# Kernel optimization log

Hardware: AMD Instinct MI355X
Metric: run time of the kernel (lower is better)

The kernel has to match this reference:

```python
import jax, jax.numpy as jnp
import numpy as np

# Module config (matches init_kwargs)
B, S, H = 4, 4096, 1024      # batch, seq_len, hidden_size
M = 2048                     # expert_dim (mid dim of each expert FFN)
E = 16                       # num_experts
K = 2                        # top_k


def setup_inputs() -> dict:
    key = jax.random.key(0)
    ks = jax.random.split(key, 5)
    X = jax.random.normal(ks[0], (B, S, H), dtype=jnp.float32)
    # gate: Linear(H, E)
    Wg = jax.random.normal(ks[1], (H, E), dtype=jnp.float32) * 0.02
    bg = jnp.zeros((E,), dtype=jnp.float32)
    # stacked expert params: fc1 (H->M), fc2 (M->H)
    W1 = jax.random.normal(ks[2], (E, H, M), dtype=jnp.float32) * 0.02
    b1 = jnp.zeros((E, M), dtype=jnp.float32)
    W2 = jax.random.normal(ks[3], (E, M, H), dtype=jnp.float32) * 0.02
    b2 = jnp.zeros((E, H), dtype=jnp.float32)
    return {"X": X, "Wg": Wg, "bg": bg, "W1": W1, "b1": b1, "W2": W2, "b2": b2}


def reference(X, Wg, bg, W1, b1, W2, b2):
    Bs, Ss, Hs = X.shape
    Xf = X.reshape(-1, Hs)                          # [T, H], T = B*S
    T = Xf.shape[0]
    # gate -> softmax -> top-k -> renormalize (same math as torch.topk(softmax))
    probs = jax.nn.softmax(Xf @ Wg + bg, axis=-1)   # [T, E]
    top_w, top_idx = jax.lax.top_k(probs, K)        # [T, K]
    top_w = top_w / jnp.sum(top_w, axis=-1, keepdims=True)
    # per-token combine weight for each expert (0 if expert not selected)
    cw = jnp.zeros((T, E), dtype=Xf.dtype).at[jnp.arange(T)[:, None], top_idx].add(top_w)  # [T, E]

    # scan over experts: each expert runs on all tokens, masked by its combine weight.
    # Mathematically identical to the per-token loop: out[t] = sum_k w[t,k] * Expert[idx[t,k]](x[t])
    def body(acc, xs):
        w1, bb1, w2, bb2, g = xs                    # g: [T] combine weights for this expert
        h = jax.nn.relu(Xf @ w1 + bb1)              # [T, M]
        acc = acc + g[:, None] * (h @ w2 + bb2)     # [T, H]
        return acc, None

    out, _ = jax.lax.scan(body, jnp.zeros_like(Xf), (W1, b1, W2, b2, cw.T))
    return out.reshape(Bs, Ss, Hs)
```

## Files before the change

kernel.cpp:

```cpp
#include <hip/hip_runtime.h>
#include <stdint.h>

#define T_TOK 16384
#define H_DIM 1024
#define M_DIM 2048
#define E_NUM 16

typedef __attribute__((ext_vector_type(8))) short bf16x8;
typedef __attribute__((ext_vector_type(4))) float f32x4;

#define GLOAD_LDS16(g, l) __builtin_amdgcn_global_load_lds( \
    (const __attribute__((address_space(1))) void*)(g),     \
    (__attribute__((address_space(3))) void*)(l), 16, 0, 0)

__device__ __forceinline__ ushort f2b(float f){ union{float f; unsigned i;} v; v.f=f; unsigned r=(v.i + 0x7fffu + ((v.i>>16)&1u))>>16; return (ushort)r; }

__global__ void k_detect(const ushort* X, int* flag){
  if (threadIdx.x == 0){
    int huge = 0;
    for (int i = 0; i < 256; i++){
      int ex = (X[i] >> 7) & 0xff;
      if (ex >= 200) huge = 1;
    }
    flag[0] = huge;
  }
}

__global__ void k_zero_fb(ushort* out, int n){
  int i = blockIdx.x * 256 + threadIdx.x;
  if (i < n) out[i] = 0;
}

__global__ __launch_bounds__(256) void k_zero(char* out, const int* flag, size_t half){
  size_t i = ((size_t)blockIdx.x * 256 + threadIdx.x) * 16;
  *(uint4*)(out + i) = make_uint4(0u,0u,0u,0u);
  if (flag[0] == 1) *(uint4*)(out + half + i) = make_uint4(0u,0u,0u,0u);
}

__global__ __launch_bounds__(256) void k_gate(const float* __restrict__ X,
    const float* __restrict__ Wg, const float* __restrict__ bg,
    float* __restrict__ top_w, int* __restrict__ pick,
    ushort* __restrict__ Xb, const int* __restrict__ flag)
{
  if (flag[0] != 1) return;
  int wave = threadIdx.x >> 6, lane = threadIdx.x & 63;
  int t0 = (blockIdx.x * 4 + wave) * 4;
  int equad = lane & 3, hgrp = lane >> 2;

  const float* x0 = X + (size_t)t0 * H_DIM;
  const float* x1 = x0 + H_DIM;
  const float* x2 = x1 + H_DIM;
  const float* x3 = x2 + H_DIM;

  float4 a0 = make_float4(0.f,0.f,0.f,0.f);
  float4 a1 = make_float4(0.f,0.f,0.f,0.f);
  float4 a2 = make_float4(0.f,0.f,0.f,0.f);
  float4 a3 = make_float4(0.f,0.f,0.f,0.f);

  #pragma unroll 4
  for (int hb = 0; hb < H_DIM / 16; hb++){
    int h = hb * 16 + hgrp;
    float4 w = *(const float4*)(Wg + h * E_NUM + equad * 4);
    float v0 = x0[h], v1 = x1[h], v2 = x2[h], v3 = x3[h];
    a0.x = fmaf(v0, w.x, a0.x); a0.y = fmaf(v0, w.y, a0.y); a0.z = fmaf(v0, w.z, a0.z); a0.w = fmaf(v0, w.w, a0.w);
    a1.x = fmaf(v1, w.x, a1.x); a1.y = fmaf(v1, w.y, a1.y); a1.z = fmaf(v1, w.z, a1.z); a1.w = fmaf(v1, w.w, a1.w);
    a2.x = fmaf(v2, w.x, a2.x); a2.y = fmaf(v2, w.y, a2.y); a2.z = fmaf(v2, w.z, a2.z); a2.w = fmaf(v2, w.w, a2.w);
    a3.x = fmaf(v3, w.x, a3.x); a3.y = fmaf(v3, w.y, a3.y); a3.z = fmaf(v3, w.z, a3.z); a3.w = fmaf(v3, w.w, a3.w);
  }

  #pragma unroll
  for (int off = 4; off <= 32; off <<= 1){
    a0.x += __shfl_xor(a0.x, off, 64); a0.y += __shfl_xor(a0.y, off, 64);
    a0.z += __shfl_xor(a0.z, off, 64); a0.w += __shfl_xor(a0.w, off, 64);
    a1.x += __shfl_xor(a1.x, off, 64); a1.y += __shfl_xor(a1.y, off, 64);
    a1.z += __shfl_xor(a1.z, off, 64); a1.w += __shfl_xor(a1.w, off, 64);
    a2.x += __shfl_xor(a2.x, off, 64); a2.y += __shfl_xor(a2.y, off, 64);
    a2.z += __shfl_xor(a2.z, off, 64); a2.w += __shfl_xor(a2.w, off, 64);
    a3.x += __shfl_xor(a3.x, off, 64); a3.y += __shfl_xor(a3.y, off, 64);
    a3.z += __shfl_xor(a3.z, off, 64); a3.w += __shfl_xor(a3.w, off, 64);
  }

  float lg0[16], lg1[16], lg2[16], lg3[16];
  #pragma unroll
  for (int g = 0; g < 4; g++){
    lg0[g*4+0] = __shfl(a0.x, g, 64); lg0[g*4+1] = __shfl(a0.y, g, 64);
    lg0[g*4+2] = __shfl(a0.z, g, 64); lg0[g*4+3] = __shfl(a0.w, g, 64);
    lg1[g*4+0] = __shfl(a1.x, g, 64); lg1[g*4+1] = __shfl(a1.y, g, 64);
    lg1[g*4+2] = __shfl(a1.z, g, 64); lg1[g*4+3] = __shfl(a1.w, g, 64);
    lg2[g*4+0] = __shfl(a2.x, g, 64); lg2[g*4+1] = __shfl(a2.y, g, 64);
    lg2[g*4+2] = __shfl(a2.z, g, 64); lg2[g*4+3] = __shfl(a2.w, g, 64);
    lg3[g*4+0] = __shfl(a3.x, g, 64); lg3[g*4+1] = __shfl(a3.y, g, 64);
    lg3[g*4+2] = __shfl(a3.z, g, 64); lg3[g*4+3] = __shfl(a3.w, g, 64);
  }
  #pragma unroll
  for (int e = 0; e < E_NUM; e++){
    float b = bg[e];
    lg0[e] += b; lg1[e] += b; lg2[e] += b; lg3[e] += b;
  }

  if (lane == 0){
    #pragma unroll
    for (int tk = 0; tk < 4; tk++){
      const float* lg = (tk == 0) ? lg0 : (tk == 1) ? lg1 : (tk == 2) ? lg2 : lg3;
      int t = t0 + tk;
      int i1 = 0; float m1 = lg[0];
      #pragma unroll
      for (int e = 1; e < E_NUM; e++) if (lg[e] > m1){ m1 = lg[e]; i1 = e; }
      int i2 = -1; float m2 = -1e30f;
      #pragma unroll
      for (int e = 0; e < E_NUM; e++) if (e != i1 && lg[e] > m2){ m2 = lg[e]; i2 = e; }
      if (i2 < 0) i2 = (i1 + 1) & 15;
      float e2 = __expf(m2 - m1);
      float w1 = 1.f / (1.f + e2);
      top_w[t*2]   = w1;
      top_w[t*2+1] = 1.f - w1;
      pick[t] = i1 | (i2 << 8);
    }
  }

  #pragma unroll
  for (int tk = 0; tk < 4; tk++){
    const float* xr = X + (size_t)(t0 + tk) * H_DIM;
    ushort* xb = Xb + (size_t)(t0 + tk) * H_DIM;
    #pragma unroll
    for (int hb = 0; hb < 4; hb++){
      int idx = hb * 256 + lane * 4;
      float4 v = *(const float4*)(xr + idx);
      ushort4 u;
      u.x = f2b(v.x); u.y = f2b(v.y); u.z = f2b(v.z); u.w = f2b(v.w);
      *(ushort4*)(xb + idx) = u;
    }
  }
}

__global__ __launch_bounds__(256) void k_bucket(const int* __restrict__ pick,
    int* __restrict__ cnt, int* __restrict__ bucket, const int* __restrict__ flag)
{
  if (flag[0] != 1) return;
  int e = blockIdx.x;
  int tid = threadIdx.x, lane = tid & 63, wave = tid >> 6;
  __shared__ int wsum[4];
  int running = 0;
  for (int c0 = 0; c0 < T_TOK; c0 += 256){
    int t = c0 + tid;
    int pk = pick[t];
    int val = -1;
    if ((pk & 0xff) == e) val = t * 2;
    else if (((pk >> 8) & 0xff) == e) val = t * 2 + 1;
    unsigned long long m = __ballot(val >= 0);
    int myidx = __popcll(m & ((1ull << lane) - 1ull));
    if (lane == 0) wsum[wave] = __popcll(m);
    __syncthreads();
    int wbase = 0;
    #pragma unroll
    for (int w = 0; w < 4; w++) if (w < wave) wbase += wsum[w];
    int tot = wsum[0] + wsum[1] + wsum[2] + wsum[3];
    if (val >= 0) bucket[e * T_TOK + running + wbase + myidx] = val;
    running += tot;
    __syncthreads();
  }
  if (tid == 0) cnt[e] = running;
}

__global__ void k_sched(const int* cnt, int* scan, int* ntl, int2* desc, const int* flag){
  if (threadIdx.x == 0){
    if (flag[0] != 1){ ntl[0] = 0; return; }
    int rowacc = 0, tot = 0;
    for (int e = 0; e < E_NUM; e++){
      scan[e] = rowacc; int c = cnt[e]; rowacc += c;
      int nt = (c + 127) >> 7;
      for (int t = 0; t < nt && tot < 384; t++){ desc[tot] = make_int2(e, t); tot++; }
    }
    ntl[0] = tot;
  }
}

__global__ __launch_bounds__(256) void k_transpose_cvt(const float* __restrict__ src,
                                                       ushort* __restrict__ dst,
                                                       int R, int C, const int* flag)
{
  if (flag[0] != 1) return;
  __shared__ ushort tile[64][68];
  int e = blockIdx.z;
  src += (size_t)e * R * C; dst += (size_t)e * R * C;
  int c0 = blockIdx.x * 64, r0 = blockIdx.y * 64;
  int tc = (threadIdx.x & 15) * 4, tr = threadIdx.x >> 4;
  #pragma unroll
  for (int p = 0; p < 4; p++){
    int r = tr + p * 16;
    float4 v = *(const float4*)&src[(size_t)(r0 + r) * C + (c0 + tc)];
    tile[r][tc] = f2b(v.x); tile[r][tc+1] = f2b(v.y); tile[r][tc+2] = f2b(v.z); tile[r][tc+3] = f2b(v.w);
  }
  __syncthreads();
  #pragma unroll
  for (int p = 0; p < 4; p++){
    int c = tr + p * 16;
    ushort4 v;
    v.x = tile[tc+0][c]; v.y = tile[tc+1][c]; v.z = tile[tc+2][c]; v.w = tile[tc+3][c];
    *(ushort4*)&dst[(size_t)(c0 + c) * R + (r0 + tc)] = v;
  }
}

__global__ __launch_bounds__(256) void k_fc1(
    const ushort* __restrict__ X, const ushort* __restrict__ W1t,
    const float* __restrict__ b1, ushort* __restrict__ h,
    const int* __restrict__ cnt, const int* __restrict__ scan,
    const int* __restrict__ ntl, const int2* __restrict__ desc,
    const int* __restrict__ bucket)
{
  if ((int)blockIdx.y >= ntl[0]) return;
  int2 d = desc[blockIdx.y];
  int e = d.x, tIdx = d.y;
  int c = cnt[e], sE = scan[e];
  int row0 = tIdx * 128, n0 = blockIdx.x * 128;

  __shared__ ushort As[128 * 64];
  __shared__ ushort Bs[128 * 64];
  __shared__ int rowTok[128];

  int tid = threadIdx.x, lane = tid & 63, wave = tid >> 6;
  if (tid < 128){
    int i = row0 + tid; int ic = i < c ? i : c - 1;
    rowTok[tid] = bucket[e * T_TOK + ic] >> 1;
  }
  __syncthreads();

  const char* aBase[4]; const char* bBase[4];
  #pragma unroll
  for (int cc = 0; cc < 4; cc++){
    int chunk = wave * 256 + cc * 64 + lane;
    int r = chunk >> 3, j = chunk & 7, jd = j ^ (r & 7);
    int tok = rowTok[r];
    aBase[cc] = (const char*)X + ((size_t)tok * H_DIM) * 2 + jd * 16;
    bBase[cc] = (const char*)W1t + ((size_t)(e * M_DIM + n0 + r) * H_DIM) * 2 + jd * 16;
  }

  f32x4 acc[4][4];
  #pragma unroll
  for (int mt = 0; mt < 4; mt++)
    #pragma unroll
    for (int nt = 0; nt < 4; nt++) acc[mt][nt] = (f32x4){0.f, 0.f, 0.f, 0.f};

  int wm = (wave >> 1) * 64, wn = (wave & 1) * 64;
  int col = lane & 15, quad = lane >> 4;

  for (int k0 = 0; k0 < H_DIM; k0 += 64){
    #pragma unroll
    for (int cc = 0; cc < 4; cc++){
      GLOAD_LDS16(aBase[cc] + k0 * 2, As + (wave * 256 + cc * 64) * 8);
      GLOAD_LDS16(bBase[cc] + k0 * 2, Bs + (wave * 256 + cc * 64) * 8);
    }
    __syncthreads();
    #pragma unroll
    for (int ks = 0; ks < 2; ks++){
      int jdA = (ks * 4 + quad) ^ (col & 7);
      bf16x8 af[4], bfr[4];
      #pragma unroll
      for (int mt = 0; mt < 4; mt++)
        af[mt] = *(const bf16x8*)&As[(wm + mt * 16 + col) * 64 + jdA * 8];
      #pragma unroll
      for (int nt = 0; nt < 4; nt++)
        bfr[nt] = *(const bf16x8*)&Bs[(wn + nt * 16 + col) * 64 + jdA * 8];
      #pragma unroll
      for (int mt = 0; mt < 4; mt++)
        #pragma unroll
        for (int nt = 0; nt < 4; nt++)
          acc[mt][nt] = __builtin_amdgcn_mfma_f32_16x16x32_bf16(af[mt], bfr[nt], acc[mt][nt], 0, 0, 0);
    }
    __syncthreads();
  }

  float bias[4];
  #pragma unroll
  for (int nt = 0; nt < 4; nt++) bias[nt] = b1[e * M_DIM + n0 + wn + nt * 16 + col];
  #pragma unroll
  for (int mt = 0; mt < 4; mt++){
    #pragma unroll
    for (int reg = 0; reg < 4; reg++){
      int ml = wm + mt * 16 + quad * 4 + reg;
      int i = row0 + ml;
      if (i < c){
        size_t base = (size_t)(sE + i) * M_DIM + n0 + wn + col;
        #pragma unroll
        for (int nt = 0; nt < 4; nt++){
          float v = acc[mt][nt][reg] + bias[nt];
          v = v > 0.f ? v : 0.f;
          h[base + nt * 16] = f2b(v);
        }
      }
    }
  }
}

__global__ __launch_bounds__(256) void k_fc2(
    const ushort* __restrict__ hbuf, const ushort* __restrict__ W2t,
    const float* __restrict__ b2, const float* __restrict__ top_w,
    float* __restrict__ out,
    const int* __restrict__ cnt, const int* __restrict__ scan,
    const int* __restrict__ ntl, const int2* __restrict__ desc,
    const int* __restrict__ bucket)
{
  if ((int)blockIdx.y >= ntl[0]) return;
  int2 d = desc[blockIdx.y];
  int e = d.x, tIdx = d.y;
  int c = cnt[e], sE = scan[e];
  int row0 = tIdx * 128, n0 = blockIdx.x * 128;

  __shared__ ushort As[128 * 64];
  __shared__ ushort Bs[128 * 64];
  __shared__ int rowLds[128];
  __shared__ float wLds[128];

  int tid = threadIdx.x, lane = tid & 63, wave = tid >> 6;
  if (tid < 128){
    int i = row0 + tid; int ic = i < c ? i : c - 1;
    int pk = bucket[e * T_TOK + ic];
    rowLds[tid] = pk >> 1; wLds[tid] = top_w[pk];
  }
  __syncthreads();

  const char* aBase[4]; const char* bBase[4];
  #pragma unroll
  for (int cc = 0; cc < 4; cc++){
    int chunk = wave * 256 + cc * 64 + lane;
    int r = chunk >> 3, j = chunk & 7, jd = j ^ (r & 7);
    int i = row0 + r; int ic = i < c ? i : c - 1;
    aBase[cc] = (const char*)hbuf + ((size_t)(sE + ic) * M_DIM) * 2 + jd * 16;
    bBase[cc] = (const char*)W2t + ((size_t)(e * H_DIM + n0 + r) * M_DIM) * 2 + jd * 16;
  }

  f32x4 acc[4][4];
  #pragma unroll
  for (int mt = 0; mt < 4; mt++)
    #pragma unroll
    for (int nt = 0; nt < 4; nt++) acc[mt][nt] = (f32x4){0.f, 0.f, 0.f, 0.f};

  int wm = (wave >> 1) * 64, wn = (wave & 1) * 64;
  int col = lane & 15, quad = lane >> 4;

  for (int k0 = 0; k0 < M_DIM; k0 += 64){
    #pragma unroll
    for (int cc = 0; cc < 4; cc++){
      GLOAD_LDS16(aBase[cc] + k0 * 2, As + (wave * 256 + cc * 64) * 8);
      GLOAD_LDS16(bBase[cc] + k0 * 2, Bs + (wave * 256 + cc * 64) * 8);
    }
    __syncthreads();
    #pragma unroll
    for (int ks = 0; ks < 2; ks++){
      int jdA = (ks * 4 + quad) ^ (col & 7);
      bf16x8 af[4], bfr[4];
      #pragma unroll
      for (int mt = 0; mt < 4; mt++)
        af[mt] = *(const bf16x8*)&As[(wm + mt * 16 + col) * 64 + jdA * 8];
      #pragma unroll
      for (int nt = 0; nt < 4; nt++)
        bfr[nt] = *(const bf16x8*)&Bs[(wn + nt * 16 + col) * 64 + jdA * 8];
      #pragma unroll
      for (int mt = 0; mt < 4; mt++)
        #pragma unroll
        for (int nt = 0; nt < 4; nt++)
          acc[mt][nt] = __builtin_amdgcn_mfma_f32_16x16x32_bf16(af[mt], bfr[nt], acc[mt][nt], 0, 0, 0);
    }
    __syncthreads();
  }

  float bias[4];
  #pragma unroll
  for (int nt = 0; nt < 4; nt++) bias[nt] = b2[e * H_DIM + n0 + wn + nt * 16 + col];
  #pragma unroll
  for (int mt = 0; mt < 4; mt++){
    #pragma unroll
    for (int reg = 0; reg < 4; reg++){
      int ml = wm + mt * 16 + quad * 4 + reg;
      int i = row0 + ml;
      if (i < c){
        int trow = rowLds[ml];
        float w = wLds[ml];
        size_t base = (size_t)trow * H_DIM + n0 + wn + col;
        #pragma unroll
        for (int nt = 0; nt < 4; nt++){
          float v = (acc[mt][nt][reg] + bias[nt]) * w;
          atomicAdd(&out[base + nt * 16], v);
        }
      }
    }
  }
}

extern "C" void kernel_launch(void* const* d_in, const int* in_sizes, int n_in,
                              void* d_out, int out_size, void* d_ws, size_t ws_size,
                              hipStream_t stream)
{
  const float* X  = (const float*)d_in[0];
  const float* Wg = (const float*)d_in[1];
  const float* bg = (const float*)d_in[2];
  const float* W1 = (const float*)d_in[3];
  const float* b1 = (const float*)d_in[4];
  const float* W2 = (const float*)d_in[5];
  const float* b2 = (const float*)d_in[6];
  float* out = (float*)d_out;

  const size_t AUX_SZ  = 2097152;
  const size_t XBF_SZ  = (size_t)T_TOK * H_DIM * 2;
  const size_t HBUF_SZ = (size_t)2 * T_TOK * M_DIM * 2;
  const size_t WT_SZ   = (size_t)E_NUM * H_DIM * M_DIM * 2;
  const size_t NEEDED  = AUX_SZ + XBF_SZ + HBUF_SZ + WT_SZ;

  if (ws_size < NEEDED){
    k_zero_fb<<<(out_size + 255) / 256, 256, 0, stream>>>((ushort*)d_out, out_size);
    return;
  }

  char* ws = (char*)d_ws;
  int*  cnt    = (int*)(ws);
  int*  scan   = (int*)(ws + 256);
  int*  ntl    = (int*)(ws + 512);
  int*  flag   = (int*)(ws + 768);
  int2* desc   = (int2*)(ws + 1024);
  float* topw  = (float*)(ws + 4096);
  int*  bucket = (int*)(ws + 139264);
  int*  pick   = (int*)(ws + 1572864);
  ushort* Xbf  = (ushort*)(ws + AUX_SZ);
  ushort* hbuf = (ushort*)(ws + AUX_SZ + XBF_SZ);
  ushort* Wt   = (ushort*)(ws + AUX_SZ + XBF_SZ + HBUF_SZ);

  k_detect<<<1, 64, 0, stream>>>((const ushort*)d_in[0], flag);
  k_zero<<<out_size / 2048, 256, 0, stream>>>((char*)d_out, flag, (size_t)out_size * 2);
  k_gate<<<1024, 256, 0, stream>>>(X, Wg, bg, topw, pick, Xbf, flag);
  k_bucket<<<E_NUM, 256, 0, stream>>>(pick, cnt, bucket, flag);
  k_sched<<<1, 64, 0, stream>>>(cnt, scan, ntl, desc, flag);
  k_transpose_cvt<<<dim3(32, 16, 16), 256, 0, stream>>>(W1, Wt, 1024, 2048, flag);
  k_fc1<<<dim3(16, 272), 256, 0, stream>>>(Xbf, Wt, b1, hbuf, cnt, scan, ntl, desc, bucket);
  k_transpose_cvt<<<dim3(16, 32, 16), 256, 0, stream>>>(W2, Wt, 2048, 1024, flag);
  k_fc2<<<dim3(8, 272), 256, 0, stream>>>(hbuf, Wt, b2, topw, out, cnt, scan, ntl, desc, bucket);
}
```

Baseline: 979.2 us.

## Double-buffer LDS tiles in expert GEMMs to overlap global loads with MFMA

Both expert GEMM kernels now use two LDS buffers per operand and prefetch the next K-slice with global_load_lds while MFMAs run on the current slice, with one waitcnt plus barrier per iteration. This targets the load latency that the single-buffer loop exposed between its two syncthreads. The per-block row index and weight LDS tables are removed: token indices and combine weights are now read directly from global memory per thread. LDS use doubles to 64KB per block, which may lower occupancy, and the direct gathers add redundant global reads.

```diff
diff --git a/kernel.cpp b/kernel.cpp
--- a/kernel.cpp
+++ b/kernel.cpp
@@ -214,23 +214,20 @@
   int c = cnt[e], sE = scan[e];
   int row0 = tIdx * 128, n0 = blockIdx.x * 128;
 
-  __shared__ ushort As[128 * 64];
-  __shared__ ushort Bs[128 * 64];
-  __shared__ int rowTok[128];
+  __shared__ ushort As[2][128 * 64];
+  __shared__ ushort Bs[2][128 * 64];
 
   int tid = threadIdx.x, lane = tid & 63, wave = tid >> 6;
-  if (tid < 128){
-    int i = row0 + tid; int ic = i < c ? i : c - 1;
-    rowTok[tid] = bucket[e * T_TOK + ic] >> 1;
-  }
-  __syncthreads();
 
   const char* aBase[4]; const char* bBase[4];
+  int ldsOff[4];
   #pragma unroll
   for (int cc = 0; cc < 4; cc++){
     int chunk = wave * 256 + cc * 64 + lane;
     int r = chunk >> 3, j = chunk & 7, jd = j ^ (r & 7);
-    int tok = rowTok[r];
+    int i = row0 + r; int ic = i < c ? i : c - 1;
+    int tok = bucket[e * T_TOK + ic] >> 1;
+    ldsOff[cc] = chunk * 8;
     aBase[cc] = (const char*)X + ((size_t)tok * H_DIM) * 2 + jd * 16;
     bBase[cc] = (const char*)W1t + ((size_t)(e * M_DIM + n0 + r) * H_DIM) * 2 + jd * 16;
   }
@@ -244,30 +241,43 @@
   int wm = (wave >> 1) * 64, wn = (wave & 1) * 64;
   int col = lane & 15, quad = lane >> 4;
 
+  #pragma unroll
+  for (int cc = 0; cc < 4; cc++){
+    GLOAD_LDS16(aBase[cc], &As[0][ldsOff[cc]]);
+    GLOAD_LDS16(bBase[cc], &Bs[0][ldsOff[cc]]);
+  }
+  asm volatile("s_waitcnt vmcnt(0)" ::: "memory");
+  __builtin_amdgcn_s_barrier();
+
+  int cur = 0;
   for (int k0 = 0; k0 < H_DIM; k0 += 64){
-    #pragma unroll
-    for (int cc = 0; cc < 4; cc++){
-      GLOAD_LDS16(aBase[cc] + k0 * 2, As + (wave * 256 + cc * 64) * 8);
-      GLOAD_LDS16(bBase[cc] + k0 * 2, Bs + (wave * 256 + cc * 64) * 8);
-    }
-    __syncthreads();
+    int nxt = cur ^ 1;
+    if (k0 + 64 < H_DIM){
+      #pragma unroll
+      for (int cc = 0; cc < 4; cc++){
+        GLOAD_LDS16(aBase[cc] + (k0 + 64) * 2, &As[nxt][ldsOff[cc]]);
+        GLOAD_LDS16(bBase[cc] + (k0 + 64) * 2, &Bs[nxt][ldsOff[cc]]);
+      }
+    }
     #pragma unroll
     for (int ks = 0; ks < 2; ks++){
       int jdA = (ks * 4 + quad) ^ (col & 7);
       bf16x8 af[4], bfr[4];
       #pragma unroll
       for (int mt = 0; mt < 4; mt++)
-        af[mt] = *(const bf16x8*)&As[(wm + mt * 16 + col) * 64 + jdA * 8];
+        af[mt] = *(const bf16x8*)&As[cur][(wm + mt * 16 + col) * 64 + jdA * 8];
       #pragma unroll
       for (int nt = 0; nt < 4; nt++)
-        bfr[nt] = *(const bf16x8*)&Bs[(wn + nt * 16 + col) * 64 + jdA * 8];
+        bfr[nt] = *(const bf16x8*)&Bs[cur][(wn + nt * 16 + col) * 64 + jdA * 8];
       #pragma unroll
       for (int mt = 0; mt < 4; mt++)
         #pragma unroll
         for (int nt = 0; nt < 4; nt++)
           acc[mt][nt] = __builtin_amdgcn_mfma_f32_16x16x32_bf16(af[mt], bfr[nt], acc[mt][nt], 0, 0, 0);
     }
-    __syncthreads();
+    asm volatile("s_waitcnt vmcnt(0)" ::: "memory");
+    __builtin_amdgcn_s_barrier();
+    cur = nxt;
   }
 
   float bias[4];
@@ -306,25 +316,19 @@
   int c = cnt[e], sE = scan[e];
   int row0 = tIdx * 128, n0 = blockIdx.x * 128;
 
-  __shared__ ushort As[128 * 64];
-  __shared__ ushort Bs[128 * 64];
-  __shared__ int rowLds[128];
-  __shared__ float wLds[128];
+  __shared__ ushort As[2][128 * 64];
+  __shared__ ushort Bs[2][128 * 64];
 
   int tid = threadIdx.x, lane = tid & 63, wave = tid >> 6;
-  if (tid < 128){
-    int i = row0 + tid; int ic = i < c ? i : c - 1;
-    int pk = bucket[e * T_TOK + ic];
-    rowLds[tid] = pk >> 1; wLds[tid] = top_w[pk];
-  }
-  __syncthreads();
 
   const char* aBase[4]; const char* bBase[4];
+  int ldsOff[4];
   #pragma unroll
   for (int cc = 0; cc < 4; cc++){
     int chunk = wave * 256 + cc * 64 + lane;
     int r = chunk >> 3, j = chunk & 7, jd = j ^ (r & 7);
     int i = row0 + r; int ic = i < c ? i : c - 1;
+    ldsOff[cc] = chunk * 8;
     aBase[cc] = (const char*)hbuf + ((size_t)(sE + ic) * M_DIM) * 2 + jd * 16;
     bBase[cc] = (const char*)W2t + ((size_t)(e * H_DIM + n0 + r) * M_DIM) * 2 + jd * 16;
   }
@@ -338,30 +342,43 @@
   int wm = (wave >> 1) * 64, wn = (wave & 1) * 64;
   int col = lane & 15, quad = lane >> 4;
 
+  #pragma unroll
+  for (int cc = 0; cc < 4; cc++){
+    GLOAD_LDS16(aBase[cc], &As[0][ldsOff[cc]]);
+    GLOAD_LDS16(bBase[cc], &Bs[0][ldsOff[cc]]);
+  }
+  asm volatile("s_waitcnt vmcnt(0)" ::: "memory");
+  __builtin_amdgcn_s_barrier();
+
+  int cur = 0;
   for (int k0 = 0; k0 < M_DIM; k0 += 64){
-    #pragma unroll
-    for (int cc = 0; cc < 4; cc++){
-      GLOAD_LDS16(aBase[cc] + k0 * 2, As + (wave * 256 + cc * 64) * 8);
-      GLOAD_LDS16(bBase[cc] + k0 * 2, Bs + (wave * 256 + cc * 64) * 8);
-    }
-    __syncthreads();
+    int nxt = cur ^ 1;
+    if (k0 + 64 < M_DIM){
+      #pragma unroll
+      for (int cc = 0; cc < 4; cc++){
+        GLOAD_LDS16(aBase[cc] + (k0 + 64) * 2, &As[nxt][ldsOff[cc]]);
+        GLOAD_LDS16(bBase[cc] + (k0 + 64) * 2, &Bs[nxt][ldsOff[cc]]);
+      }
+    }
     #pragma unroll
     for (int ks = 0; ks < 2; ks++){
       int jdA = (ks * 4 + quad) ^ (col & 7);
       bf16x8 af[4], bfr[4];
       #pragma unroll
       for (int mt = 0; mt < 4; mt++)
-        af[mt] = *(const bf16x8*)&As[(wm + mt * 16 + col) * 64 + jdA * 8];
+        af[mt] = *(const bf16x8*)&As[cur][(wm + mt * 16 + col) * 64 + jdA * 8];
       #pragma unroll
       for (int nt = 0; nt < 4; nt++)
-        bfr[nt] = *(const bf16x8*)&Bs[(wn + nt * 16 + col) * 64 + jdA * 8];
+        bfr[nt] = *(const bf16x8*)&Bs[cur][(wn + nt * 16 + col) * 64 + jdA * 8];
       #pragma unroll
       for (int mt = 0; mt < 4; mt++)
         #pragma unroll
         for (int nt = 0; nt < 4; nt++)
           acc[mt][nt] = __builtin_amdgcn_mfma_f32_16x16x32_bf16(af[mt], bfr[nt], acc[mt][nt], 0, 0, 0);
     }
-    __syncthreads();
+    asm volatile("s_waitcnt vmcnt(0)" ::: "memory");
+    __builtin_amdgcn_s_barrier();
+    cur = nxt;
   }
 
   float bias[4];
@@ -374,8 +391,9 @@
       int ml = wm + mt * 16 + quad * 4 + reg;
       int i = row0 + ml;
       if (i < c){
-        int trow = rowLds[ml];
-        float w = wLds[ml];
+        int pk = bucket[e * T_TOK + i];
+        int trow = pk >> 1;
+        float w = top_w[pk];
         size_t base = (size_t)trow * H_DIM + n0 + wn + col;
         #pragma unroll
         for (int nt = 0; nt < 4; nt++){
```

After: 958.2 us. -2.1%, faster.
